# Optimization experiments

Measured on AMD Instinct MI355X. Metric: run time of the kernel, lower is better.

The kernel has to match this reference:

```python
import jax, jax.numpy as jnp
import numpy as np

N = 8192          # num_nodes
E = 262144        # num_edges = N * avg_degree(32)
K_SIGN = 1000.0   # ExactModel k
EPSILON = 5.0     # ExactModel epsilon


def setup_inputs() -> dict:
    key = jax.random.key(0)
    k1, k2, k3, k4 = jax.random.split(key, 4)
    src = jax.random.randint(k1, (E,), 0, N)
    dst = jax.random.randint(k2, (E,), 0, N)
    edge_index = jnp.stack([src, dst]).astype(jnp.int32)          # (2, E)
    # partition vector, elements in {1, ..., N}
    p = jax.random.randint(k3, (N,), 1, N + 1).astype(jnp.float32)  # (N,)
    x = jax.random.normal(k4, (N, 1), dtype=jnp.float32)            # node features
    return {"edge_index": edge_index, "p": p, "x": x}


def reference(edge_index, p, x):
    """infoco1 (segment logsumexp over edges with self-loops) followed by one
    refine step: pairwise difference matrix + CustomSignFunction tanh + row-sum."""
    n = p.shape[0]
    log_n = jnp.log(jnp.asarray(n, dtype=p.dtype))
    loops = jnp.arange(n, dtype=edge_index.dtype)
    src = jnp.concatenate([edge_index[0], loops])   # add_self_loops
    dst = jnp.concatenate([edge_index[1], loops])
    # contributions_log = log(p_i) + p_j * log(N)
    contrib = jnp.log(p[src]) + p[dst] * log_n      # (E + N,)
    # numerically stable segment log-sum-exp over incoming edges of each node
    mx = jax.ops.segment_max(contrib, dst, num_segments=n)              # scatter_max
    se = jax.ops.segment_sum(jnp.exp(contrib - mx[dst]), dst, num_segments=n)  # scatter_add
    S = mx + jnp.log(se) + jnp.dot(x[:, 0], p)      # infoco1: S_log + <x, p>
    # refine: all-pairs sign refinement, D_1 = tanh(k * (X - X^T) - eps)
    X = S[:, None]                                   # (N, 1)
    D1 = jnp.tanh(K_SIGN * (X - X.T) - EPSILON)      # (N, N)
    return D1.sum(axis=1)                            # (N,)
```

## Files before the change

kernel.cpp:

```cpp
#include <hip/hip_runtime.h>
#include <math.h>

#define K_SIGN 1000.0f
#define EPSILON 5.0f

#define D_HI ((EPSILON + 12.0f) / K_SIGN)
#define D_LO ((EPSILON - 12.0f) / K_SIGN)

#define NB_HIST 64


__global__ void __launch_bounds__(256) k_hist(
        const int* __restrict__ src, const int* __restrict__ dst,
        const float* __restrict__ p, const float* __restrict__ x,
        int* __restrict__ Hpriv, double* __restrict__ C,
        int* __restrict__ PFX, int* __restrict__ pos, int e, int n) {
    __shared__ int buf[8192];
    __shared__ int csum[256];
    __shared__ double dred[4];
    int tid = threadIdx.x;
    int b = blockIdx.x;

    int4* b4 = (int4*)buf;
    for (int i = tid; i < n / 4; i += 256) b4[i] = make_int4(0, 0, 0, 0);
    __syncthreads();

    if (b < NB_HIST) {
        int per = (e + NB_HIST - 1) / NB_HIST;
        int t0 = b * per;
        int t1 = min(t0 + per, e);
        for (int t = t0 + tid; t < t1; t += 256)
            atomicAdd(&buf[dst[t]], (int)p[src[t]]);
        __syncthreads();
        int4* o4 = (int4*)(Hpriv + b * n);
        for (int i = tid; i < n / 4; i += 256) o4[i] = b4[i];
        return;
    }

    double acc = 0.0;
    for (int i = tid; i < n; i += 256) {
        float pv = p[i];
        atomicAdd(&buf[(int)pv - 1], 1);
        acc += (double)x[i] * (double)pv;
    }
    for (int off = 32; off > 0; off >>= 1)
        acc += __shfl_down(acc, off, 64);
    if ((tid & 63) == 0) dred[tid >> 6] = acc;
    __syncthreads();
    if (tid == 0) *C = dred[0] + dred[1] + dred[2] + dred[3];

    int cw = n / 256;
    int base = tid * cw;
    int s = 0;
    for (int k = 0; k < cw; ++k) s += buf[base + k];
    csum[tid] = s;
    __syncthreads();
    for (int off = 1; off < 256; off <<= 1) {
        int v = (tid >= off) ? csum[tid - off] : 0;
        __syncthreads();
        csum[tid] += v;
        __syncthreads();
    }
    int run = (tid == 0) ? 0 : csum[tid - 1];
    for (int k = 0; k < cw; ++k) {
        int h = buf[base + k];
        PFX[base + k] = run;
        pos[base + k] = run;
        run += h;
    }
    if (tid == 0) PFX[n] = n;
}

__global__ void __launch_bounds__(256) k_merge(
        const int* __restrict__ Hpriv, const float* __restrict__ p,
        const double* __restrict__ C, float* __restrict__ S,
        int* __restrict__ pos, int* __restrict__ order, int n, float log_n) {
    int i = blockIdx.x * 256 + threadIdx.x;
    if (i >= n) return;
    float pv = p[i];
    int t = (int)pv;
#pragma unroll 8
    for (int b = 0; b < NB_HIST; ++b) t += Hpriv[b * n + i];
    S[i] = (logf((float)t) + pv * log_n) + (float)(*C);
    int r = atomicAdd(&pos[(int)pv - 1], 1);
    order[r] = i;
}

__global__ void __launch_bounds__(256) k_out(const float* __restrict__ S,
                                             const float* __restrict__ p,
                                             const int* __restrict__ PFX,
                                             const int* __restrict__ order,
                                             float* __restrict__ out, int n) {
    int i = blockIdx.x * 256 + threadIdx.x;
    if (i >= n) return;
    int pi = (int)p[i];
    int base = PFX[pi - 1];
    int g = PFX[pi] - base;
    float si = S[i];
    float acc = (float)(base - (n - base - g));
    for (int k = 0; k < g; ++k) {
        int j = order[base + k];
        float d = si - S[j];
        if (d > D_HI) acc += 1.0f;
        else if (d < D_LO) acc -= 1.0f;
        else acc += tanhf(fmaf(K_SIGN, d, -EPSILON));
    }
    out[i] = acc;
}

extern "C" void kernel_launch(void* const* d_in, const int* in_sizes, int n_in,
                              void* d_out, int out_size, void* d_ws, size_t ws_size,
                              hipStream_t stream) {
    const int* edge_index = (const int*)d_in[0];
    const float* p = (const float*)d_in[1];
    const float* x = (const float*)d_in[2];
    float* out = (float*)d_out;

    int e = in_sizes[0] / 2;
    int n = in_sizes[1];
    const int* src = edge_index;
    const int* dst = edge_index + e;

    double* C = (double*)d_ws;
    float* S = (float*)((char*)d_ws + 16);
    int* PFX = (int*)(S + n);
    int* pos = PFX + (n + 4);
    int* order = pos + n;
    int* Hpriv = order + n;

    float log_n = logf((float)n);

    k_hist<<<NB_HIST + 1, 256, 0, stream>>>(src, dst, p, x, Hpriv, C,
                                            PFX, pos, e, n);
    k_merge<<<n / 256, 256, 0, stream>>>(Hpriv, p, C, S, pos, order, n, log_n);
    k_out<<<n / 256, 256, 0, stream>>>(S, p, PFX, order, out, n);
}
```

Measured before the change: 86.73 us.

## Build order buckets in shared memory and split histogram merge across waves

Counting-sort scatter of node indices into the order array moves from global atomics in k_merge into the single histogram-prefix block, using shared-memory atomics on the prefix buffer. k_merge now processes 64 nodes per block, with four wavefronts each summing 16 private histograms and reducing through shared memory, giving more parallel loads per node. k_out runs with 64-thread blocks to spread nodes over more CUs. The trade-off is extra serial work in the one prefix block of k_hist.

```diff
diff --git a/kernel.cpp b/kernel.cpp
--- a/kernel.cpp
+++ b/kernel.cpp
@@ -14,7 +14,7 @@
         const int* __restrict__ src, const int* __restrict__ dst,
         const float* __restrict__ p, const float* __restrict__ x,
         int* __restrict__ Hpriv, double* __restrict__ C,
-        int* __restrict__ PFX, int* __restrict__ pos, int e, int n) {
+        int* __restrict__ PFX, int* __restrict__ order, int e, int n) {
     __shared__ int buf[8192];
     __shared__ int csum[256];
     __shared__ double dred[4];
@@ -65,33 +65,44 @@
     for (int k = 0; k < cw; ++k) {
         int h = buf[base + k];
         PFX[base + k] = run;
-        pos[base + k] = run;
+        buf[base + k] = run;
         run += h;
     }
     if (tid == 0) PFX[n] = n;
+    __syncthreads();
+
+    for (int i = tid; i < n; i += 256) {
+        int r = atomicAdd(&buf[(int)p[i] - 1], 1);
+        order[r] = i;
+    }
 }
 
 __global__ void __launch_bounds__(256) k_merge(
         const int* __restrict__ Hpriv, const float* __restrict__ p,
         const double* __restrict__ C, float* __restrict__ S,
-        int* __restrict__ pos, int* __restrict__ order, int n, float log_n) {
-    int i = blockIdx.x * 256 + threadIdx.x;
-    if (i >= n) return;
-    float pv = p[i];
-    int t = (int)pv;
-#pragma unroll 8
-    for (int b = 0; b < NB_HIST; ++b) t += Hpriv[b * n + i];
-    S[i] = (logf((float)t) + pv * log_n) + (float)(*C);
-    int r = atomicAdd(&pos[(int)pv - 1], 1);
-    order[r] = i;
+        int n, float log_n) {
+    __shared__ int part[4][64];
+    int q = threadIdx.x >> 6;
+    int l = threadIdx.x & 63;
+    int i = blockIdx.x * 64 + l;
+    int s = 0;
+#pragma unroll
+    for (int b = q * 16; b < q * 16 + 16; ++b) s += Hpriv[b * n + i];
+    part[q][l] = s;
+    __syncthreads();
+    if (q == 0) {
+        float pv = p[i];
+        int t = (int)pv + part[0][l] + part[1][l] + part[2][l] + part[3][l];
+        S[i] = (logf((float)t) + pv * log_n) + (float)(*C);
+    }
 }
 
-__global__ void __launch_bounds__(256) k_out(const float* __restrict__ S,
-                                             const float* __restrict__ p,
-                                             const int* __restrict__ PFX,
-                                             const int* __restrict__ order,
-                                             float* __restrict__ out, int n) {
-    int i = blockIdx.x * 256 + threadIdx.x;
+__global__ void __launch_bounds__(64) k_out(const float* __restrict__ S,
+                                            const float* __restrict__ p,
+                                            const int* __restrict__ PFX,
+                                            const int* __restrict__ order,
+                                            float* __restrict__ out, int n) {
+    int i = blockIdx.x * 64 + threadIdx.x;
     if (i >= n) return;
     int pi = (int)p[i];
     int base = PFX[pi - 1];
@@ -124,14 +135,13 @@
     double* C = (double*)d_ws;
     float* S = (float*)((char*)d_ws + 16);
     int* PFX = (int*)(S + n);
-    int* pos = PFX + (n + 4);
-    int* order = pos + n;
+    int* order = PFX + (n + 4);
     int* Hpriv = order + n;
 
     float log_n = logf((float)n);
 
     k_hist<<<NB_HIST + 1, 256, 0, stream>>>(src, dst, p, x, Hpriv, C,
-                                            PFX, pos, e, n);
-    k_merge<<<n / 256, 256, 0, stream>>>(Hpriv, p, C, S, pos, order, n, log_n);
-    k_out<<<n / 256, 256, 0, stream>>>(S, p, PFX, order, out, n);
+                                            PFX, order, e, n);
+    k_merge<<<n / 64, 256, 0, stream>>>(Hpriv, p, C, S, n, log_n);
+    k_out<<<n / 64, 64, 0, stream>>>(S, p, PFX, order, out, n);
 }
```

Result: slower. 95.58 us (+10.2%).
